# Performance work log

Measured on AMD Instinct MI355X. Metric: run time of the kernel, lower is better.

## Reference

```python
import jax, jax.numpy as jnp
import numpy as np

N = 262144      # total line-graph nodes (16 graphs x 16384)
E = 2097152     # total line-graph edges (avg degree 8)
F_IN = 8        # edge_attr feature dim
FEATURES_DIM = 64


def gcn_conv(x, src, dst, W, b, n):
    """PyG GCNConv: x' = D^{-1/2} (A+I) D^{-1/2} (x W) + b, deg from in-edges incl. self-loops."""
    x = x @ W
    loop = jnp.arange(n, dtype=src.dtype)
    si = jnp.concatenate([src, loop])
    di = jnp.concatenate([dst, loop])
    deg = jax.ops.segment_sum(jnp.ones(si.shape[0], dtype=x.dtype), di, num_segments=n)
    dinv = jnp.where(deg > 0, deg ** -0.5, 0.0)
    norm = dinv[si] * dinv[di]                      # [E+N]
    msg = x[si] * norm[:, None]                     # gather + scale
    return jax.ops.segment_sum(msg, di, num_segments=n) + b


def setup_inputs() -> dict:
    key = jax.random.key(0)
    ks = jax.random.split(key, 10)

    def lin(k, fan_in, fan_out):
        return jax.random.normal(k, (fan_in, fan_out), jnp.float32) * (1.0 / np.sqrt(fan_in))

    return {
        "x": jax.random.normal(ks[0], (N, F_IN), jnp.float32),
        "W1": lin(ks[1], F_IN, 16), "b1": jnp.zeros((16,), jnp.float32),
        "W2": lin(ks[2], 16, 32),   "b2": jnp.zeros((32,), jnp.float32),
        "W3": lin(ks[3], 32, 64),   "b3": jnp.zeros((64,), jnp.float32),
        "Wfc": lin(ks[4], 64, FEATURES_DIM), "bfc": jnp.zeros((FEATURES_DIM,), jnp.float32),
        "edge_index": jax.random.randint(ks[5], (2, E), 0, N, dtype=jnp.int32),
        "batch_size": 16,
    }


def reference(x, W1, b1, W2, b2, W3, b3, Wfc, bfc, edge_index, batch_size):
    src, dst = edge_index[0], edge_index[1]
    n = x.shape[0]
    h = jax.nn.relu(gcn_conv(x, src, dst, W1, b1, n))
    h = jax.nn.relu(gcn_conv(h, src, dst, W2, b2, n))
    h = jax.nn.relu(gcn_conv(h, src, dst, W3, b3, n))
    out = h @ Wfc + bfc
    return out.reshape(batch_size, -1, FEATURES_DIM)
```

## Files before the change

kernel.cpp:

```cpp
#include <hip/hip_runtime.h>
#include <hip/hip_bf16.h>


#define NB   256
#define NPB  1024
#define TILE 4096
#define SRCMASK 0x3FFFFu

typedef _Float16 half8 __attribute__((ext_vector_type(8)));
typedef float float4v __attribute__((ext_vector_type(4)));

__device__ __forceinline__ unsigned pkh(float a, float b) {
    unsigned short ua = __builtin_bit_cast(unsigned short, (_Float16)a);
    unsigned short ub = __builtin_bit_cast(unsigned short, (_Float16)b);
    return (unsigned)ua | ((unsigned)ub << 16);
}
__device__ __forceinline__ float h_lo(unsigned u) {
    return (float)__builtin_bit_cast(_Float16, (unsigned short)(u & 0xFFFFu));
}
__device__ __forceinline__ float h_hi(unsigned u) {
    return (float)__builtin_bit_cast(_Float16, (unsigned short)(u >> 16));
}

#define UNPK8_ADD(A, u) \
    A##0 += h_lo(u.x); A##1 += h_hi(u.x); A##2 += h_lo(u.y); A##3 += h_hi(u.y); \
    A##4 += h_lo(u.z); A##5 += h_hi(u.z); A##6 += h_lo(u.w); A##7 += h_hi(u.w);

__global__ void hist_kernel(const int* __restrict__ dst, int* __restrict__ ghist,
                            int E, int shift) {
    __shared__ int h[NB];
    int tid = threadIdx.x;
    h[tid] = 0;
    __syncthreads();
    int base = blockIdx.x * TILE;
    int cnt = min(TILE, E - base);
    for (int i = tid; i < cnt; i += 256)
        atomicAdd(&h[dst[base + i] >> shift], 1);
    __syncthreads();
    int v = h[tid];
    if (v) atomicAdd(&ghist[tid], v);
}

__global__ void bscan_kernel(const int* __restrict__ ghist, int* __restrict__ bbase,
                             int* __restrict__ gcursor,
                             const float* __restrict__ W3, const float* __restrict__ Wf,
                             _Float16* __restrict__ w3f, _Float16* __restrict__ wff) {
    __shared__ int sh[NB];
    int tid = threadIdx.x;
    int v = ghist[tid];
    sh[tid] = v;
    __syncthreads();
    for (int o = 1; o < NB; o <<= 1) {
        int t = (tid >= o) ? sh[tid - o] : 0;
        __syncthreads();
        sh[tid] += t;
        __syncthreads();
    }
    int incl = sh[tid];
    bbase[tid] = incl - v;
    gcursor[tid] = incl - v;
    if (tid == NB - 1) bbase[NB] = incl;
    for (int i = tid; i < 32 * 64; i += NB) {
        int k = i >> 6, j = i & 63;
        w3f[(j >> 4) * 512 + (j & 15) * 32 + (k >> 3) * 8 + (k & 7)] = (_Float16)W3[i];
    }
    for (int i = tid; i < 64 * 64; i += NB) {
        int k = i >> 6, j = i & 63;
        wff[((k >> 5) * 4 + (j >> 4)) * 512 + (j & 15) * 32 + ((k >> 3) & 3) * 8 + (k & 7)]
            = (_Float16)Wf[i];
    }
}

__global__ void __launch_bounds__(256)
partition_kernel(const int* __restrict__ src, const int* __restrict__ dst,
                 int* __restrict__ gcursor, unsigned int* __restrict__ bedge,
                 int E, int shift, int mask) {
    __shared__ int h[NB], st[NB], gp[NB];
    __shared__ unsigned short rk[TILE];
    __shared__ int sd[TILE];
    __shared__ int ss[TILE];
    int tid = threadIdx.x;
    h[tid] = 0;
    __syncthreads();
    int base = blockIdx.x * TILE;
    int cnt = min(TILE, E - base);
    for (int i = tid; i < cnt; i += 256)
        rk[i] = (unsigned short)atomicAdd(&h[dst[base + i] >> shift], 1);
    __syncthreads();
    int hv = h[tid];
    st[tid] = hv;
    __syncthreads();
    for (int o = 1; o < NB; o <<= 1) {
        int t = (tid >= o) ? st[tid - o] : 0;
        __syncthreads();
        st[tid] += t;
        __syncthreads();
    }
    st[tid] -= hv;
    gp[tid] = hv ? atomicAdd(&gcursor[tid], hv) : 0;
    __syncthreads();
    for (int i = tid; i < cnt; i += 256) {
        int d = dst[base + i];
        int b = d >> shift;
        int pos = st[b] + rk[i];
        sd[pos] = d;
        ss[pos] = src[base + i];
    }
    __syncthreads();
    for (int i = tid; i < cnt; i += 256) {
        int d = sd[i];
        int b = d >> shift;
        int g = gp[b] + (i - st[b]);
        bedge[g] = (unsigned int)ss[i] | ((unsigned int)(d & mask) << 18);
    }
}

__global__ void __launch_bounds__(256)
build_kernel(const int* __restrict__ bbase, const unsigned int* __restrict__ bedge,
             const float* __restrict__ x,
             int* __restrict__ off, float* __restrict__ dinv, int* __restrict__ adj,
             _Float16* __restrict__ y0h) {
    __shared__ int deg1[NPB];
    __shared__ int cur[NPB];
    __shared__ int bs[256];
    int tid = threadIdx.x;
    int b = blockIdx.x;
    int s = bbase[b], e = bbase[b + 1];
    int base = tid * 4;
#pragma unroll
    for (int i = 0; i < 4; i++) deg1[base + i] = 0;
    __syncthreads();
    for (int i = s + tid; i < e; i += 256)
        atomicAdd(&deg1[bedge[i] >> 18], 1);
    __syncthreads();
    int d0 = deg1[base], d1 = deg1[base + 1], d2 = deg1[base + 2], d3 = deg1[base + 3];
    int th = d0 + d1 + d2 + d3;
    bs[tid] = th;
    __syncthreads();
    for (int o = 1; o < 256; o <<= 1) {
        int t = (tid >= o) ? bs[tid - o] : 0;
        __syncthreads();
        bs[tid] += t;
        __syncthreads();
    }
    int run = s + bs[tid] - th;
    int vb = b * NPB + base;
    off[vb]     = run; cur[base]     = run; dinv[vb]     = rsqrtf((float)(d0 + 1)); run += d0;
    off[vb + 1] = run; cur[base + 1] = run; dinv[vb + 1] = rsqrtf((float)(d1 + 1)); run += d1;
    off[vb + 2] = run; cur[base + 2] = run; dinv[vb + 2] = rsqrtf((float)(d2 + 1)); run += d2;
    off[vb + 3] = run; cur[base + 3] = run; dinv[vb + 3] = rsqrtf((float)(d3 + 1)); run += d3;
    if (b == NB - 1 && tid == 255) off[NB * NPB] = e;
    __syncthreads();
    for (int i = s + tid; i < e; i += 256) {
        unsigned int pk = bedge[i];
        int p = atomicAdd(&cur[pk >> 18], 1);
        adj[p] = (int)(pk & SRCMASK);
    }
    for (int i = tid; i < NPB; i += 256) {
        float dv = rsqrtf((float)(deg1[i] + 1));
        const float4* xr = (const float4*)x + (size_t)(b * NPB + i) * 2;
        float4 t0 = xr[0], t1 = xr[1];
        uint4 pk;
        pk.x = pkh(t0.x * dv, t0.y * dv); pk.y = pkh(t0.z * dv, t0.w * dv);
        pk.z = pkh(t1.x * dv, t1.y * dv); pk.w = pkh(t1.z * dv, t1.w * dv);
        ((uint4*)y0h)[(size_t)b * NPB + i] = pk;
    }
}

__global__ void __launch_bounds__(256)
aggt1_kernel(const _Float16* __restrict__ y0h, const int* __restrict__ off,
             const int* __restrict__ adj, const float* __restrict__ dinv,
             const float* __restrict__ W1, const float* __restrict__ b1,
             _Float16* __restrict__ y1h) {
    __shared__ float Ws[8 * 16];
    __shared__ float bsh[16];
    const int tid = threadIdx.x;
    if (tid < 128) Ws[tid] = W1[tid];
    if (tid < 16) bsh[tid] = b1[tid];
    const int vg = blockIdx.x * 256 + tid;
    const uint4* y4 = (const uint4*)y0h;
    int beg = off[vg], end = off[vg + 1];
    uint4 us = y4[vg];
    float a0 = h_lo(us.x), a1 = h_hi(us.x), a2 = h_lo(us.y), a3 = h_hi(us.y),
          a4 = h_lo(us.z), a5 = h_hi(us.z), a6 = h_lo(us.w), a7 = h_hi(us.w);
    float c0 = 0, c1 = 0, c2 = 0, c3 = 0, c4 = 0, c5 = 0, c6 = 0, c7 = 0;
    int e = beg;
    for (; e + 8 <= end; e += 8) {
        int s0 = adj[e], s1 = adj[e + 1], s2 = adj[e + 2], s3 = adj[e + 3];
        int s4 = adj[e + 4], s5 = adj[e + 5], s6 = adj[e + 6], s7 = adj[e + 7];
        uint4 u0 = y4[s0], u1 = y4[s1], u2 = y4[s2], u3 = y4[s3];
        uint4 u4 = y4[s4], u5 = y4[s5], u6 = y4[s6], u7 = y4[s7];
        UNPK8_ADD(a, u0) UNPK8_ADD(c, u1) UNPK8_ADD(a, u2) UNPK8_ADD(c, u3)
        UNPK8_ADD(a, u4) UNPK8_ADD(c, u5) UNPK8_ADD(a, u6) UNPK8_ADD(c, u7)
    }
    for (; e + 2 <= end; e += 2) {
        int s0 = adj[e], s1 = adj[e + 1];
        uint4 u0 = y4[s0], u1 = y4[s1];
        UNPK8_ADD(a, u0) UNPK8_ADD(c, u1)
    }
    if (e < end) {
        uint4 u0 = y4[adj[e]];
        UNPK8_ADD(a, u0)
    }
    float dv = dinv[vg];
    float in[8];
    in[0] = (a0 + c0) * dv; in[1] = (a1 + c1) * dv;
    in[2] = (a2 + c2) * dv; in[3] = (a3 + c3) * dv;
    in[4] = (a4 + c4) * dv; in[5] = (a5 + c5) * dv;
    in[6] = (a6 + c6) * dv; in[7] = (a7 + c7) * dv;
    __syncthreads();
    const float4* W4 = (const float4*)Ws;
    float o[16];
    {
        float4 b0 = ((const float4*)bsh)[0], b1v = ((const float4*)bsh)[1];
        float4 b2v = ((const float4*)bsh)[2], b3v = ((const float4*)bsh)[3];
        o[0] = b0.x; o[1] = b0.y; o[2] = b0.z; o[3] = b0.w;
        o[4] = b1v.x; o[5] = b1v.y; o[6] = b1v.z; o[7] = b1v.w;
        o[8] = b2v.x; o[9] = b2v.y; o[10] = b2v.z; o[11] = b2v.w;
        o[12] = b3v.x; o[13] = b3v.y; o[14] = b3v.z; o[15] = b3v.w;
    }
#pragma unroll
    for (int k = 0; k < 8; k++) {
        float xk = in[k];
        float4 w0 = W4[k * 4 + 0], w1 = W4[k * 4 + 1];
        float4 w2 = W4[k * 4 + 2], w3 = W4[k * 4 + 3];
        o[0] = fmaf(xk, w0.x, o[0]);  o[1] = fmaf(xk, w0.y, o[1]);
        o[2] = fmaf(xk, w0.z, o[2]);  o[3] = fmaf(xk, w0.w, o[3]);
        o[4] = fmaf(xk, w1.x, o[4]);  o[5] = fmaf(xk, w1.y, o[5]);
        o[6] = fmaf(xk, w1.z, o[6]);  o[7] = fmaf(xk, w1.w, o[7]);
        o[8] = fmaf(xk, w2.x, o[8]);  o[9] = fmaf(xk, w2.y, o[9]);
        o[10] = fmaf(xk, w2.z, o[10]); o[11] = fmaf(xk, w2.w, o[11]);
        o[12] = fmaf(xk, w3.x, o[12]); o[13] = fmaf(xk, w3.y, o[13]);
        o[14] = fmaf(xk, w3.z, o[14]); o[15] = fmaf(xk, w3.w, o[15]);
    }
    uint4 p0, p1;
    p0.x = pkh(dv * fmaxf(o[0], 0.f),  dv * fmaxf(o[1], 0.f));
    p0.y = pkh(dv * fmaxf(o[2], 0.f),  dv * fmaxf(o[3], 0.f));
    p0.z = pkh(dv * fmaxf(o[4], 0.f),  dv * fmaxf(o[5], 0.f));
    p0.w = pkh(dv * fmaxf(o[6], 0.f),  dv * fmaxf(o[7], 0.f));
    p1.x = pkh(dv * fmaxf(o[8], 0.f),  dv * fmaxf(o[9], 0.f));
    p1.y = pkh(dv * fmaxf(o[10], 0.f), dv * fmaxf(o[11], 0.f));
    p1.z = pkh(dv * fmaxf(o[12], 0.f), dv * fmaxf(o[13], 0.f));
    p1.w = pkh(dv * fmaxf(o[14], 0.f), dv * fmaxf(o[15], 0.f));
    uint4* out4 = (uint4*)y1h;
    out4[(size_t)vg * 2]     = p0;
    out4[(size_t)vg * 2 + 1] = p1;
}

__global__ void __launch_bounds__(256)
aggt2_kernel(const _Float16* __restrict__ y1h, const int* __restrict__ off,
             const int* __restrict__ adj, const float* __restrict__ dinv,
             const float* __restrict__ W2, const float* __restrict__ b2,
             unsigned int* __restrict__ y2b) {
    __shared__ float Ws[16 * 32];
    __shared__ float bsh[32];
    const int tid = threadIdx.x;
    for (int i = tid; i < 16 * 32; i += 256) Ws[i] = W2[i];
    if (tid < 32) bsh[tid] = b2[tid];
    const int vbase = blockIdx.x * 128;
    const int vl = tid >> 1, c = tid & 1;
    const int vg = vbase + vl;
    const uint4* y4 = (const uint4*)y1h;
    int beg = off[vg], end = off[vg + 1];
    uint4 us = y4[(size_t)vg * 2 + c];
    float a0 = h_lo(us.x), a1 = h_hi(us.x), a2 = h_lo(us.y), a3 = h_hi(us.y),
          a4 = h_lo(us.z), a5 = h_hi(us.z), a6 = h_lo(us.w), a7 = h_hi(us.w);
    float c0 = 0, c1 = 0, c2 = 0, c3 = 0, c4 = 0, c5 = 0, c6 = 0, c7 = 0;
    int e = beg;
    for (; e + 8 <= end; e += 8) {
        int s0 = adj[e], s1 = adj[e + 1], s2 = adj[e + 2], s3 = adj[e + 3];
        int s4 = adj[e + 4], s5 = adj[e + 5], s6 = adj[e + 6], s7 = adj[e + 7];
        uint4 u0 = y4[(size_t)s0 * 2 + c], u1 = y4[(size_t)s1 * 2 + c];
        uint4 u2 = y4[(size_t)s2 * 2 + c], u3 = y4[(size_t)s3 * 2 + c];
        uint4 u4 = y4[(size_t)s4 * 2 + c], u5 = y4[(size_t)s5 * 2 + c];
        uint4 u6 = y4[(size_t)s6 * 2 + c], u7 = y4[(size_t)s7 * 2 + c];
        UNPK8_ADD(a, u0) UNPK8_ADD(c, u1) UNPK8_ADD(a, u2) UNPK8_ADD(c, u3)
        UNPK8_ADD(a, u4) UNPK8_ADD(c, u5) UNPK8_ADD(a, u6) UNPK8_ADD(c, u7)
    }
    for (; e + 2 <= end; e += 2) {
        int s0 = adj[e], s1 = adj[e + 1];
        uint4 u0 = y4[(size_t)s0 * 2 + c], u1 = y4[(size_t)s1 * 2 + c];
        UNPK8_ADD(a, u0) UNPK8_ADD(c, u1)
    }
    if (e < end) {
        uint4 u0 = y4[(size_t)adj[e] * 2 + c];
        UNPK8_ADD(a, u0)
    }
    float dv = dinv[vg];
    float own[8];
    own[0] = (a0 + c0) * dv; own[1] = (a1 + c1) * dv;
    own[2] = (a2 + c2) * dv; own[3] = (a3 + c3) * dv;
    own[4] = (a4 + c4) * dv; own[5] = (a5 + c5) * dv;
    own[6] = (a6 + c6) * dv; own[7] = (a7 + c7) * dv;
    float oth[8];
#pragma unroll
    for (int k = 0; k < 8; k++) oth[k] = __shfl_xor(own[k], 1);
    float in[16];
#pragma unroll
    for (int k = 0; k < 8; k++) {
        in[c * 8 + k] = own[k];
        in[(1 - c) * 8 + k] = oth[k];
    }
    __syncthreads();
    const int j0 = c * 16;
    const float4* W4 = (const float4*)Ws;
    float o[16];
#pragma unroll
    for (int jj = 0; jj < 16; jj += 4) {
        float4 bv = *(const float4*)&bsh[j0 + jj];
        o[jj] = bv.x; o[jj + 1] = bv.y; o[jj + 2] = bv.z; o[jj + 3] = bv.w;
    }
#pragma unroll
    for (int k = 0; k < 16; k++) {
        float xk = in[k];
        float4 w0 = W4[k * 8 + c * 4 + 0], w1 = W4[k * 8 + c * 4 + 1];
        float4 w2 = W4[k * 8 + c * 4 + 2], w3 = W4[k * 8 + c * 4 + 3];
        o[0] = fmaf(xk, w0.x, o[0]);  o[1] = fmaf(xk, w0.y, o[1]);
        o[2] = fmaf(xk, w0.z, o[2]);  o[3] = fmaf(xk, w0.w, o[3]);
        o[4] = fmaf(xk, w1.x, o[4]);  o[5] = fmaf(xk, w1.y, o[5]);
        o[6] = fmaf(xk, w1.z, o[6]);  o[7] = fmaf(xk, w1.w, o[7]);
        o[8] = fmaf(xk, w2.x, o[8]);  o[9] = fmaf(xk, w2.y, o[9]);
        o[10] = fmaf(xk, w2.z, o[10]); o[11] = fmaf(xk, w2.w, o[11]);
        o[12] = fmaf(xk, w3.x, o[12]); o[13] = fmaf(xk, w3.y, o[13]);
        o[14] = fmaf(xk, w3.z, o[14]); o[15] = fmaf(xk, w3.w, o[15]);
    }
    uint4 p0, p1;
    p0.x = pkh(dv * fmaxf(o[0], 0.f),  dv * fmaxf(o[1], 0.f));
    p0.y = pkh(dv * fmaxf(o[2], 0.f),  dv * fmaxf(o[3], 0.f));
    p0.z = pkh(dv * fmaxf(o[4], 0.f),  dv * fmaxf(o[5], 0.f));
    p0.w = pkh(dv * fmaxf(o[6], 0.f),  dv * fmaxf(o[7], 0.f));
    p1.x = pkh(dv * fmaxf(o[8], 0.f),  dv * fmaxf(o[9], 0.f));
    p1.y = pkh(dv * fmaxf(o[10], 0.f), dv * fmaxf(o[11], 0.f));
    p1.z = pkh(dv * fmaxf(o[12], 0.f), dv * fmaxf(o[13], 0.f));
    p1.w = pkh(dv * fmaxf(o[14], 0.f), dv * fmaxf(o[15], 0.f));
    uint4* out4 = (uint4*)y2b;
    out4[(size_t)vg * 4 + c * 2]     = p0;
    out4[(size_t)vg * 4 + c * 2 + 1] = p1;
}

__global__ void __launch_bounds__(256)
agg3_kernel(const unsigned int* __restrict__ y2b, const int* __restrict__ off,
            const int* __restrict__ adj, const float* __restrict__ dinv,
            _Float16* __restrict__ a3out, int n) {
    int t = blockIdx.x * 256 + threadIdx.x;
    int v = t >> 2, c = t & 3;
    if (v >= n) return;
    const uint4* yb = (const uint4*)y2b;
    uint4 us = yb[(size_t)v * 4 + c];
    float a0 = h_lo(us.x), a1 = h_hi(us.x), a2 = h_lo(us.y), a3 = h_hi(us.y),
          a4 = h_lo(us.z), a5 = h_hi(us.z), a6 = h_lo(us.w), a7 = h_hi(us.w);
    float c0 = 0, c1 = 0, c2 = 0, c3 = 0, c4 = 0, c5 = 0, c6 = 0, c7 = 0;
    int beg = off[v], end = off[v + 1];
    int e = beg;
    for (; e + 4 <= end; e += 4) {
        int s0 = adj[e], s1 = adj[e + 1], s2 = adj[e + 2], s3 = adj[e + 3];
        uint4 u0 = yb[(size_t)s0 * 4 + c];
        uint4 u1 = yb[(size_t)s1 * 4 + c];
        uint4 u2 = yb[(size_t)s2 * 4 + c];
        uint4 u3 = yb[(size_t)s3 * 4 + c];
        UNPK8_ADD(a, u0) UNPK8_ADD(c, u1) UNPK8_ADD(a, u2) UNPK8_ADD(c, u3)
    }
    for (; e + 2 <= end; e += 2) {
        int s0 = adj[e], s1 = adj[e + 1];
        uint4 u0 = yb[(size_t)s0 * 4 + c];
        uint4 u1 = yb[(size_t)s1 * 4 + c];
        UNPK8_ADD(a, u0) UNPK8_ADD(c, u1)
    }
    if (e < end) {
        uint4 u0 = yb[(size_t)adj[e] * 4 + c];
        UNPK8_ADD(a, u0)
    }
    float dv = dinv[v];
    uint4 st;
    st.x = pkh((a0 + c0) * dv, (a1 + c1) * dv);
    st.y = pkh((a2 + c2) * dv, (a3 + c3) * dv);
    st.z = pkh((a4 + c4) * dv, (a5 + c5) * dv);
    st.w = pkh((a6 + c6) * dv, (a7 + c7) * dv);
    ((uint4*)a3out)[(size_t)v * 4 + c] = st;
}

__global__ void __launch_bounds__(256)
t3fc_kernel(const _Float16* __restrict__ a3h,
            const _Float16* __restrict__ w3f, const float* __restrict__ b3,
            const _Float16* __restrict__ wff, const float* __restrict__ bf,
            float* __restrict__ out) {
    __shared__ __align__(16) _Float16 tA[4][1024];
    const int tid = threadIdx.x;
    const int w = tid >> 6, l = tid & 63;
    const int lr = l & 15, lh = l >> 4;
    const int vbase = blockIdx.x * 64 + w * 16;
    const int fragoff = lr * 32 + lh * 8;

    half8 A1 = *(const half8*)(a3h + (size_t)(vbase + lr) * 32 + lh * 8);

    float4v c1[4];
#pragma unroll
    for (int nt = 0; nt < 4; nt++) {
        float bv = b3[nt * 16 + lr];
        float4v ci = {bv, bv, bv, bv};
        half8 B = *(const half8*)(w3f + nt * 512 + fragoff);
        c1[nt] = __builtin_amdgcn_mfma_f32_16x16x32_f16(A1, B, ci, 0, 0, 0);
    }

    _Float16* tw = tA[w];
#pragma unroll
    for (int nt = 0; nt < 4; nt++) {
        int k2 = nt * 16 + lr;
        int base = (k2 >> 5) * 512 + ((k2 >> 3) & 3) * 8 + (k2 & 7);
#pragma unroll
        for (int r = 0; r < 4; r++)
            tw[base + (lh * 4 + r) * 32] = (_Float16)fmaxf(c1[nt][r], 0.f);
    }

    float4v c2[4];
#pragma unroll
    for (int nt = 0; nt < 4; nt++) {
        float bv = bf[nt * 16 + lr];
        c2[nt] = (float4v){bv, bv, bv, bv};
    }
#pragma unroll
    for (int ks = 0; ks < 2; ks++) {
        half8 A2 = *(const half8*)(tw + ks * 512 + fragoff);
#pragma unroll
        for (int nt = 0; nt < 4; nt++) {
            half8 B = *(const half8*)(wff + (ks * 4 + nt) * 512 + fragoff);
            c2[nt] = __builtin_amdgcn_mfma_f32_16x16x32_f16(A2, B, c2[nt], 0, 0, 0);
        }
    }

#pragma unroll
    for (int nt = 0; nt < 4; nt++) {
#pragma unroll
        for (int r = 0; r < 4; r++)
            out[(size_t)(vbase + lh * 4 + r) * 64 + nt * 16 + lr] = c2[nt][r];
    }
}

extern "C" void kernel_launch(void* const* d_in, const int* in_sizes, int n_in,
                              void* d_out, int out_size, void* d_ws, size_t ws_size,
                              hipStream_t stream) {
    const float* x  = (const float*)d_in[0];
    const float* W1 = (const float*)d_in[1];
    const float* b1 = (const float*)d_in[2];
    const float* W2 = (const float*)d_in[3];
    const float* b2 = (const float*)d_in[4];
    const float* W3 = (const float*)d_in[5];
    const float* b3 = (const float*)d_in[6];
    const float* Wf = (const float*)d_in[7];
    const float* bf = (const float*)d_in[8];
    const int*   ei = (const int*)d_in[9];

    const int N = in_sizes[0] / 8;
    const int E = in_sizes[9] / 2;
    const int* srcv = ei;
    const int* dstv = ei + E;
    const int shift = 10;

    char* p = (char*)d_ws;
    auto take = [&p](size_t bytes) { char* q = p; p += (bytes + 63) & ~size_t(63); return q; };
    int*   off   = (int*)take((size_t)(N + 16) * 4);
    float* dinv  = (float*)take((size_t)N * 4);
    int*   adj   = (int*)take((size_t)E * 4);
    int*   ghist = (int*)take(NB * 4);
    int*   bbase = (int*)take((NB + 1) * 4);
    int*   gcur  = (int*)take(NB * 4);
    _Float16* w3f = (_Float16*)take(32 * 64 * 2);
    _Float16* wff = (_Float16*)take(64 * 64 * 2);
    char*  bufA  = take((size_t)N * 32 * 4);
    char*  bufB  = take((size_t)N * 16 * 4);
    char*  regX  = take((size_t)N * 32 * 2);
    unsigned int* bedge = (unsigned int*)regX;
    unsigned int* y2b   = (unsigned int*)regX;
    _Float16* y0h = (_Float16*)bufA;
    _Float16* a3h = (_Float16*)bufA;
    _Float16* y1h = (_Float16*)bufB;

    hipMemsetAsync(ghist, 0, NB * 4, stream);

    int nt = (E + TILE - 1) / TILE;
    hist_kernel<<<nt, 256, 0, stream>>>(dstv, ghist, E, shift);
    bscan_kernel<<<1, NB, 0, stream>>>(ghist, bbase, gcur, W3, Wf, w3f, wff);
    partition_kernel<<<nt, 256, 0, stream>>>(srcv, dstv, gcur, bedge, E, shift, NPB - 1);
    build_kernel<<<NB, 256, 0, stream>>>(bbase, bedge, x, off, dinv, adj, y0h);

    aggt1_kernel<<<N / 256, 256, 0, stream>>>(y0h, off, adj, dinv, W1, b1, y1h);
    aggt2_kernel<<<N / 128, 256, 0, stream>>>(y1h, off, adj, dinv, W2, b2, y2b);
    agg3_kernel<<<(N * 4) / 256, 256, 0, stream>>>(y2b, off, adj, dinv, a3h, N);
    t3fc_kernel<<<N / 64, 256, 0, stream>>>(a3h, w3f, b3, wff, bf, (float*)d_out);
}
```

Before: 283.0 us.

## Sort nodes by in-degree to balance aggregation work across wavefront lanes

Builds a degree histogram during CSR construction, scans it, and scatters a degree-sorted permutation of nodes along with permuted offsets and dinv. The three aggregation kernels and the final MLP kernel then process nodes in degree order, so lanes in a wavefront run loops of similar length and diverge less. In exchange it adds two small kernels, extra indirection through perm, and scattered output writes. Reads of each node's own features also become non-contiguous.

```diff
diff --git a/kernel.cpp b/kernel.cpp
--- a/kernel.cpp
+++ b/kernel.cpp
@@ -6,6 +6,7 @@
 #define NPB  1024
 #define TILE 4096
 #define SRCMASK 0x3FFFFu
+#define DB   64
 
 typedef _Float16 half8 __attribute__((ext_vector_type(8)));
 typedef float float4v __attribute__((ext_vector_type(4)));
@@ -42,11 +43,12 @@
 }
 
 __global__ void bscan_kernel(const int* __restrict__ ghist, int* __restrict__ bbase,
-                             int* __restrict__ gcursor,
+                             int* __restrict__ gcursor, int* __restrict__ dhist,
                              const float* __restrict__ W3, const float* __restrict__ Wf,
                              _Float16* __restrict__ w3f, _Float16* __restrict__ wff) {
     __shared__ int sh[NB];
     int tid = threadIdx.x;
+    if (tid < DB) dhist[tid] = 0;
     int v = ghist[tid];
     sh[tid] = v;
     __syncthreads();
@@ -119,21 +121,25 @@
 build_kernel(const int* __restrict__ bbase, const unsigned int* __restrict__ bedge,
              const float* __restrict__ x,
              int* __restrict__ off, float* __restrict__ dinv, int* __restrict__ adj,
-             _Float16* __restrict__ y0h) {
+             _Float16* __restrict__ y0h, int* __restrict__ dhist) {
     __shared__ int deg1[NPB];
     __shared__ int cur[NPB];
     __shared__ int bs[256];
+    __shared__ int dh[DB];
     int tid = threadIdx.x;
     int b = blockIdx.x;
     int s = bbase[b], e = bbase[b + 1];
     int base = tid * 4;
 #pragma unroll
     for (int i = 0; i < 4; i++) deg1[base + i] = 0;
+    if (tid < DB) dh[tid] = 0;
     __syncthreads();
     for (int i = s + tid; i < e; i += 256)
         atomicAdd(&deg1[bedge[i] >> 18], 1);
     __syncthreads();
     int d0 = deg1[base], d1 = deg1[base + 1], d2 = deg1[base + 2], d3 = deg1[base + 3];
+    atomicAdd(&dh[min(d0, DB - 1)], 1); atomicAdd(&dh[min(d1, DB - 1)], 1);
+    atomicAdd(&dh[min(d2, DB - 1)], 1); atomicAdd(&dh[min(d3, DB - 1)], 1);
     int th = d0 + d1 + d2 + d3;
     bs[tid] = th;
     __syncthreads();
@@ -150,6 +156,7 @@
     off[vb + 2] = run; cur[base + 2] = run; dinv[vb + 2] = rsqrtf((float)(d2 + 1)); run += d2;
     off[vb + 3] = run; cur[base + 3] = run; dinv[vb + 3] = rsqrtf((float)(d3 + 1)); run += d3;
     if (b == NB - 1 && tid == 255) off[NB * NPB] = e;
+    if (tid < DB && dh[tid]) atomicAdd(&dhist[tid], dh[tid]);
     __syncthreads();
     for (int i = s + tid; i < e; i += 256) {
         unsigned int pk = bedge[i];
@@ -167,9 +174,55 @@
     }
 }
 
-__global__ void __launch_bounds__(256)
-aggt1_kernel(const _Float16* __restrict__ y0h, const int* __restrict__ off,
-             const int* __restrict__ adj, const float* __restrict__ dinv,
+__global__ void dscan_kernel(const int* __restrict__ dhist, int* __restrict__ dcur) {
+    __shared__ int sh[DB];
+    int tid = threadIdx.x;
+    int v = dhist[tid];
+    sh[tid] = v;
+    __syncthreads();
+    for (int o = 1; o < DB; o <<= 1) {
+        int t = (tid >= o) ? sh[tid - o] : 0;
+        __syncthreads();
+        sh[tid] += t;
+        __syncthreads();
+    }
+    dcur[tid] = sh[tid] - v;
+}
+
+__global__ void __launch_bounds__(256)
+dscatter_kernel(const int* __restrict__ off, const float* __restrict__ dinv,
+                int* __restrict__ dcur, int* __restrict__ perm,
+                uint2* __restrict__ offp, float* __restrict__ dinvp) {
+    __shared__ unsigned short rk[1024];
+    __shared__ unsigned char dgs[1024];
+    __shared__ int lh[DB], gb[DB];
+    const int tid = threadIdx.x;
+    const int vb = blockIdx.x * 1024;
+    if (tid < DB) lh[tid] = 0;
+    __syncthreads();
+    for (int ln = tid; ln < 1024; ln += 256) {
+        int v = vb + ln;
+        int d = min(off[v + 1] - off[v], DB - 1);
+        dgs[ln] = (unsigned char)d;
+        rk[ln] = (unsigned short)atomicAdd(&lh[d], 1);
+    }
+    __syncthreads();
+    if (tid < DB) gb[tid] = lh[tid] ? atomicAdd(&dcur[tid], lh[tid]) : 0;
+    __syncthreads();
+    for (int ln = tid; ln < 1024; ln += 256) {
+        int v = vb + ln;
+        int g = gb[dgs[ln]] + rk[ln];
+        perm[g] = v;
+        uint2 oo; oo.x = (unsigned)off[v]; oo.y = (unsigned)off[v + 1];
+        offp[g] = oo;
+        dinvp[g] = dinv[v];
+    }
+}
+
+__global__ void __launch_bounds__(256)
+aggt1_kernel(const _Float16* __restrict__ y0h, const uint2* __restrict__ offp,
+             const int* __restrict__ adj, const float* __restrict__ dinvp,
+             const int* __restrict__ perm,
              const float* __restrict__ W1, const float* __restrict__ b1,
              _Float16* __restrict__ y1h) {
     __shared__ float Ws[8 * 16];
@@ -177,10 +230,12 @@
     const int tid = threadIdx.x;
     if (tid < 128) Ws[tid] = W1[tid];
     if (tid < 16) bsh[tid] = b1[tid];
-    const int vg = blockIdx.x * 256 + tid;
+    const int r = blockIdx.x * 256 + tid;
+    const int pv = perm[r];
+    const uint2 oo = offp[r];
     const uint4* y4 = (const uint4*)y0h;
-    int beg = off[vg], end = off[vg + 1];
-    uint4 us = y4[vg];
+    int beg = (int)oo.x, end = (int)oo.y;
+    uint4 us = y4[pv];
     float a0 = h_lo(us.x), a1 = h_hi(us.x), a2 = h_lo(us.y), a3 = h_hi(us.y),
           a4 = h_lo(us.z), a5 = h_hi(us.z), a6 = h_lo(us.w), a7 = h_hi(us.w);
     float c0 = 0, c1 = 0, c2 = 0, c3 = 0, c4 = 0, c5 = 0, c6 = 0, c7 = 0;
@@ -202,7 +257,7 @@
         uint4 u0 = y4[adj[e]];
         UNPK8_ADD(a, u0)
     }
-    float dv = dinv[vg];
+    float dv = dinvp[r];
     float in[8];
     in[0] = (a0 + c0) * dv; in[1] = (a1 + c1) * dv;
     in[2] = (a2 + c2) * dv; in[3] = (a3 + c3) * dv;
@@ -243,13 +298,14 @@
     p1.z = pkh(dv * fmaxf(o[12], 0.f), dv * fmaxf(o[13], 0.f));
     p1.w = pkh(dv * fmaxf(o[14], 0.f), dv * fmaxf(o[15], 0.f));
     uint4* out4 = (uint4*)y1h;
-    out4[(size_t)vg * 2]     = p0;
-    out4[(size_t)vg * 2 + 1] = p1;
-}
-
-__global__ void __launch_bounds__(256)
-aggt2_kernel(const _Float16* __restrict__ y1h, const int* __restrict__ off,
-             const int* __restrict__ adj, const float* __restrict__ dinv,
+    out4[(size_t)pv * 2]     = p0;
+    out4[(size_t)pv * 2 + 1] = p1;
+}
+
+__global__ void __launch_bounds__(256)
+aggt2_kernel(const _Float16* __restrict__ y1h, const uint2* __restrict__ offp,
+             const int* __restrict__ adj, const float* __restrict__ dinvp,
+             const int* __restrict__ perm,
              const float* __restrict__ W2, const float* __restrict__ b2,
              unsigned int* __restrict__ y2b) {
     __shared__ float Ws[16 * 32];
@@ -257,12 +313,13 @@
     const int tid = threadIdx.x;
     for (int i = tid; i < 16 * 32; i += 256) Ws[i] = W2[i];
     if (tid < 32) bsh[tid] = b2[tid];
-    const int vbase = blockIdx.x * 128;
     const int vl = tid >> 1, c = tid & 1;
-    const int vg = vbase + vl;
+    const int r = blockIdx.x * 128 + vl;
+    const int pv = perm[r];
+    const uint2 oo = offp[r];
     const uint4* y4 = (const uint4*)y1h;
-    int beg = off[vg], end = off[vg + 1];
-    uint4 us = y4[(size_t)vg * 2 + c];
+    int beg = (int)oo.x, end = (int)oo.y;
+    uint4 us = y4[(size_t)pv * 2 + c];
     float a0 = h_lo(us.x), a1 = h_hi(us.x), a2 = h_lo(us.y), a3 = h_hi(us.y),
           a4 = h_lo(us.z), a5 = h_hi(us.z), a6 = h_lo(us.w), a7 = h_hi(us.w);
     float c0 = 0, c1 = 0, c2 = 0, c3 = 0, c4 = 0, c5 = 0, c6 = 0, c7 = 0;
@@ -286,7 +343,7 @@
         uint4 u0 = y4[(size_t)adj[e] * 2 + c];
         UNPK8_ADD(a, u0)
     }
-    float dv = dinv[vg];
+    float dv = dinvp[r];
     float own[8];
     own[0] = (a0 + c0) * dv; own[1] = (a1 + c1) * dv;
     own[2] = (a2 + c2) * dv; own[3] = (a3 + c3) * dv;
@@ -334,23 +391,26 @@
     p1.z = pkh(dv * fmaxf(o[12], 0.f), dv * fmaxf(o[13], 0.f));
     p1.w = pkh(dv * fmaxf(o[14], 0.f), dv * fmaxf(o[15], 0.f));
     uint4* out4 = (uint4*)y2b;
-    out4[(size_t)vg * 4 + c * 2]     = p0;
-    out4[(size_t)vg * 4 + c * 2 + 1] = p1;
-}
-
-__global__ void __launch_bounds__(256)
-agg3_kernel(const unsigned int* __restrict__ y2b, const int* __restrict__ off,
-            const int* __restrict__ adj, const float* __restrict__ dinv,
+    out4[(size_t)pv * 4 + c * 2]     = p0;
+    out4[(size_t)pv * 4 + c * 2 + 1] = p1;
+}
+
+__global__ void __launch_bounds__(256)
+agg3_kernel(const unsigned int* __restrict__ y2b, const uint2* __restrict__ offp,
+            const int* __restrict__ adj, const float* __restrict__ dinvp,
+            const int* __restrict__ perm,
             _Float16* __restrict__ a3out, int n) {
     int t = blockIdx.x * 256 + threadIdx.x;
-    int v = t >> 2, c = t & 3;
-    if (v >= n) return;
+    int r = t >> 2, c = t & 3;
+    if (r >= n) return;
+    const int pv = perm[r];
+    const uint2 oo = offp[r];
     const uint4* yb = (const uint4*)y2b;
-    uint4 us = yb[(size_t)v * 4 + c];
+    uint4 us = yb[(size_t)pv * 4 + c];
     float a0 = h_lo(us.x), a1 = h_hi(us.x), a2 = h_lo(us.y), a3 = h_hi(us.y),
           a4 = h_lo(us.z), a5 = h_hi(us.z), a6 = h_lo(us.w), a7 = h_hi(us.w);
     float c0 = 0, c1 = 0, c2 = 0, c3 = 0, c4 = 0, c5 = 0, c6 = 0, c7 = 0;
-    int beg = off[v], end = off[v + 1];
+    int beg = (int)oo.x, end = (int)oo.y;
     int e = beg;
     for (; e + 4 <= end; e += 4) {
         int s0 = adj[e], s1 = adj[e + 1], s2 = adj[e + 2], s3 = adj[e + 3];
@@ -370,17 +430,17 @@
         uint4 u0 = yb[(size_t)adj[e] * 4 + c];
         UNPK8_ADD(a, u0)
     }
-    float dv = dinv[v];
+    float dv = dinvp[r];
     uint4 st;
     st.x = pkh((a0 + c0) * dv, (a1 + c1) * dv);
     st.y = pkh((a2 + c2) * dv, (a3 + c3) * dv);
     st.z = pkh((a4 + c4) * dv, (a5 + c5) * dv);
     st.w = pkh((a6 + c6) * dv, (a7 + c7) * dv);
-    ((uint4*)a3out)[(size_t)v * 4 + c] = st;
-}
-
-__global__ void __launch_bounds__(256)
-t3fc_kernel(const _Float16* __restrict__ a3h,
+    ((uint4*)a3out)[(size_t)r * 4 + c] = st;
+}
+
+__global__ void __launch_bounds__(256)
+t3fc_kernel(const _Float16* __restrict__ a3h, const int* __restrict__ perm,
             const _Float16* __restrict__ w3f, const float* __restrict__ b3,
             const _Float16* __restrict__ wff, const float* __restrict__ bf,
             float* __restrict__ out) {
@@ -408,8 +468,8 @@
         int k2 = nt * 16 + lr;
         int base = (k2 >> 5) * 512 + ((k2 >> 3) & 3) * 8 + (k2 & 7);
 #pragma unroll
-        for (int r = 0; r < 4; r++)
-            tw[base + (lh * 4 + r) * 32] = (_Float16)fmaxf(c1[nt][r], 0.f);
+        for (int rr = 0; rr < 4; rr++)
+            tw[base + (lh * 4 + rr) * 32] = (_Float16)fmaxf(c1[nt][rr], 0.f);
     }
 
     float4v c2[4];
@@ -428,11 +488,14 @@
         }
     }
 
+    int pr[4];
+#pragma unroll
+    for (int rr = 0; rr < 4; rr++) pr[rr] = perm[vbase + lh * 4 + rr];
 #pragma unroll
     for (int nt = 0; nt < 4; nt++) {
 #pragma unroll
-        for (int r = 0; r < 4; r++)
-            out[(size_t)(vbase + lh * 4 + r) * 64 + nt * 16 + lr] = c2[nt][r];
+        for (int rr = 0; rr < 4; rr++)
+            out[(size_t)pr[rr] * 64 + nt * 16 + lr] = c2[nt][rr];
     }
 }
 
@@ -464,6 +527,11 @@
     int*   ghist = (int*)take(NB * 4);
     int*   bbase = (int*)take((NB + 1) * 4);
     int*   gcur  = (int*)take(NB * 4);
+    int*   dhist = (int*)take(DB * 4);
+    int*   dcur  = (int*)take(DB * 4);
+    int*   perm  = (int*)take((size_t)N * 4);
+    uint2* offp  = (uint2*)take((size_t)N * 8);
+    float* dinvp = (float*)take((size_t)N * 4);
     _Float16* w3f = (_Float16*)take(32 * 64 * 2);
     _Float16* wff = (_Float16*)take(64 * 64 * 2);
     char*  bufA  = take((size_t)N * 32 * 4);
@@ -479,12 +547,14 @@
 
     int nt = (E + TILE - 1) / TILE;
     hist_kernel<<<nt, 256, 0, stream>>>(dstv, ghist, E, shift);
-    bscan_kernel<<<1, NB, 0, stream>>>(ghist, bbase, gcur, W3, Wf, w3f, wff);
+    bscan_kernel<<<1, NB, 0, stream>>>(ghist, bbase, gcur, dhist, W3, Wf, w3f, wff);
     partition_kernel<<<nt, 256, 0, stream>>>(srcv, dstv, gcur, bedge, E, shift, NPB - 1);
-    build_kernel<<<NB, 256, 0, stream>>>(bbase, bedge, x, off, dinv, adj, y0h);
-
-    aggt1_kernel<<<N / 256, 256, 0, stream>>>(y0h, off, adj, dinv, W1, b1, y1h);
-    aggt2_kernel<<<N / 128, 256, 0, stream>>>(y1h, off, adj, dinv, W2, b2, y2b);
-    agg3_kernel<<<(N * 4) / 256, 256, 0, stream>>>(y2b, off, adj, dinv, a3h, N);
-    t3fc_kernel<<<N / 64, 256, 0, stream>>>(a3h, w3f, b3, wff, bf, (float*)d_out);
-}
+    build_kernel<<<NB, 256, 0, stream>>>(bbase, bedge, x, off, dinv, adj, y0h, dhist);
+    dscan_kernel<<<1, DB, 0, stream>>>(dhist, dcur);
+    dscatter_kernel<<<N / 1024, 256, 0, stream>>>(off, dinv, dcur, perm, offp, dinvp);
+
+    aggt1_kernel<<<N / 256, 256, 0, stream>>>(y0h, offp, adj, dinvp, perm, W1, b1, y1h);
+    aggt2_kernel<<<N / 128, 256, 0, stream>>>(y1h, offp, adj, dinvp, perm, W2, b2, y2b);
+    agg3_kernel<<<(N * 4) / 256, 256, 0, stream>>>(y2b, offp, adj, dinvp, perm, a3h, N);
+    t3fc_kernel<<<N / 64, 256, 0, stream>>>(a3h, perm, w3f, b3, wff, bf, (float*)d_out);
+}
```

Measured after the change: 319.9 us. 13.0% more time.

## Split layer-2 aggregation into two half-feature passes with nontemporal index loads

Applied to the files above, without the earlier changes.

Layer-1 output is stored as two separate 8-half planes instead of one interleaved 16-half row. Layer-2 aggregation is split into two kernels, each gathering one plane with one thread per node. The first writes fp32 partial sums to a scratch buffer and the second combines them and applies W2. Each gather pass now touches a smaller working set that fits better in cache. The adjacency reads and several stores are made nontemporal to avoid polluting cache. The cost is a second pass over adj and an extra fp32 partial-sum round trip through memory.

```diff
diff --git a/kernel.cpp b/kernel.cpp
--- a/kernel.cpp
+++ b/kernel.cpp
@@ -9,6 +9,7 @@
 
 typedef _Float16 half8 __attribute__((ext_vector_type(8)));
 typedef float float4v __attribute__((ext_vector_type(4)));
+typedef unsigned int u32x4 __attribute__((ext_vector_type(4)));
 
 __device__ __forceinline__ unsigned pkh(float a, float b) {
     unsigned short ua = __builtin_bit_cast(unsigned short, (_Float16)a);
@@ -21,6 +22,7 @@
 __device__ __forceinline__ float h_hi(unsigned u) {
     return (float)__builtin_bit_cast(_Float16, (unsigned short)(u >> 16));
 }
+__device__ __forceinline__ int ld_nt(const int* p) { return __builtin_nontemporal_load(p); }
 
 #define UNPK8_ADD(A, u) \
     A##0 += h_lo(u.x); A##1 += h_hi(u.x); A##2 += h_lo(u.y); A##3 += h_hi(u.y); \
@@ -171,35 +173,37 @@
 aggt1_kernel(const _Float16* __restrict__ y0h, const int* __restrict__ off,
              const int* __restrict__ adj, const float* __restrict__ dinv,
              const float* __restrict__ W1, const float* __restrict__ b1,
-             _Float16* __restrict__ y1h) {
+             _Float16* __restrict__ y1a, _Float16* __restrict__ y1b) {
     __shared__ float Ws[8 * 16];
     __shared__ float bsh[16];
     const int tid = threadIdx.x;
     if (tid < 128) Ws[tid] = W1[tid];
     if (tid < 16) bsh[tid] = b1[tid];
     const int vg = blockIdx.x * 256 + tid;
-    const uint4* y4 = (const uint4*)y0h;
+    const u32x4* y4 = (const u32x4*)y0h;
     int beg = off[vg], end = off[vg + 1];
-    uint4 us = y4[vg];
+    u32x4 us = y4[vg];
     float a0 = h_lo(us.x), a1 = h_hi(us.x), a2 = h_lo(us.y), a3 = h_hi(us.y),
           a4 = h_lo(us.z), a5 = h_hi(us.z), a6 = h_lo(us.w), a7 = h_hi(us.w);
     float c0 = 0, c1 = 0, c2 = 0, c3 = 0, c4 = 0, c5 = 0, c6 = 0, c7 = 0;
     int e = beg;
     for (; e + 8 <= end; e += 8) {
-        int s0 = adj[e], s1 = adj[e + 1], s2 = adj[e + 2], s3 = adj[e + 3];
-        int s4 = adj[e + 4], s5 = adj[e + 5], s6 = adj[e + 6], s7 = adj[e + 7];
-        uint4 u0 = y4[s0], u1 = y4[s1], u2 = y4[s2], u3 = y4[s3];
-        uint4 u4 = y4[s4], u5 = y4[s5], u6 = y4[s6], u7 = y4[s7];
+        int s0 = ld_nt(adj + e),     s1 = ld_nt(adj + e + 1);
+        int s2 = ld_nt(adj + e + 2), s3 = ld_nt(adj + e + 3);
+        int s4 = ld_nt(adj + e + 4), s5 = ld_nt(adj + e + 5);
+        int s6 = ld_nt(adj + e + 6), s7 = ld_nt(adj + e + 7);
+        u32x4 u0 = y4[s0], u1 = y4[s1], u2 = y4[s2], u3 = y4[s3];
+        u32x4 u4 = y4[s4], u5 = y4[s5], u6 = y4[s6], u7 = y4[s7];
         UNPK8_ADD(a, u0) UNPK8_ADD(c, u1) UNPK8_ADD(a, u2) UNPK8_ADD(c, u3)
         UNPK8_ADD(a, u4) UNPK8_ADD(c, u5) UNPK8_ADD(a, u6) UNPK8_ADD(c, u7)
     }
     for (; e + 2 <= end; e += 2) {
-        int s0 = adj[e], s1 = adj[e + 1];
-        uint4 u0 = y4[s0], u1 = y4[s1];
+        int s0 = ld_nt(adj + e), s1 = ld_nt(adj + e + 1);
+        u32x4 u0 = y4[s0], u1 = y4[s1];
         UNPK8_ADD(a, u0) UNPK8_ADD(c, u1)
     }
     if (e < end) {
-        uint4 u0 = y4[adj[e]];
+        u32x4 u0 = y4[ld_nt(adj + e)];
         UNPK8_ADD(a, u0)
     }
     float dv = dinv[vg];
@@ -233,7 +237,7 @@
         o[12] = fmaf(xk, w3.x, o[12]); o[13] = fmaf(xk, w3.y, o[13]);
         o[14] = fmaf(xk, w3.z, o[14]); o[15] = fmaf(xk, w3.w, o[15]);
     }
-    uint4 p0, p1;
+    u32x4 p0, p1;
     p0.x = pkh(dv * fmaxf(o[0], 0.f),  dv * fmaxf(o[1], 0.f));
     p0.y = pkh(dv * fmaxf(o[2], 0.f),  dv * fmaxf(o[3], 0.f));
     p0.z = pkh(dv * fmaxf(o[4], 0.f),  dv * fmaxf(o[5], 0.f));
@@ -242,100 +246,124 @@
     p1.y = pkh(dv * fmaxf(o[10], 0.f), dv * fmaxf(o[11], 0.f));
     p1.z = pkh(dv * fmaxf(o[12], 0.f), dv * fmaxf(o[13], 0.f));
     p1.w = pkh(dv * fmaxf(o[14], 0.f), dv * fmaxf(o[15], 0.f));
-    uint4* out4 = (uint4*)y1h;
-    out4[(size_t)vg * 2]     = p0;
-    out4[(size_t)vg * 2 + 1] = p1;
-}
-
-__global__ void __launch_bounds__(256)
-aggt2_kernel(const _Float16* __restrict__ y1h, const int* __restrict__ off,
-             const int* __restrict__ adj, const float* __restrict__ dinv,
-             const float* __restrict__ W2, const float* __restrict__ b2,
-             unsigned int* __restrict__ y2b) {
+    __builtin_nontemporal_store(p0, (u32x4*)y1a + vg);
+    __builtin_nontemporal_store(p1, (u32x4*)y1b + vg);
+}
+
+__global__ void __launch_bounds__(256)
+aggt2a_kernel(const _Float16* __restrict__ y1a, const int* __restrict__ off,
+              const int* __restrict__ adj, float* __restrict__ P) {
+    const int vg = blockIdx.x * 256 + threadIdx.x;
+    const u32x4* y4 = (const u32x4*)y1a;
+    int beg = off[vg], end = off[vg + 1];
+    u32x4 us = y4[vg];
+    float a0 = h_lo(us.x), a1 = h_hi(us.x), a2 = h_lo(us.y), a3 = h_hi(us.y),
+          a4 = h_lo(us.z), a5 = h_hi(us.z), a6 = h_lo(us.w), a7 = h_hi(us.w);
+    float c0 = 0, c1 = 0, c2 = 0, c3 = 0, c4 = 0, c5 = 0, c6 = 0, c7 = 0;
+    int e = beg;
+    for (; e + 8 <= end; e += 8) {
+        int s0 = ld_nt(adj + e),     s1 = ld_nt(adj + e + 1);
+        int s2 = ld_nt(adj + e + 2), s3 = ld_nt(adj + e + 3);
+        int s4 = ld_nt(adj + e + 4), s5 = ld_nt(adj + e + 5);
+        int s6 = ld_nt(adj + e + 6), s7 = ld_nt(adj + e + 7);
+        u32x4 u0 = y4[s0], u1 = y4[s1], u2 = y4[s2], u3 = y4[s3];
+        u32x4 u4 = y4[s4], u5 = y4[s5], u6 = y4[s6], u7 = y4[s7];
+        UNPK8_ADD(a, u0) UNPK8_ADD(c, u1) UNPK8_ADD(a, u2) UNPK8_ADD(c, u3)
+        UNPK8_ADD(a, u4) UNPK8_ADD(c, u5) UNPK8_ADD(a, u6) UNPK8_ADD(c, u7)
+    }
+    for (; e + 2 <= end; e += 2) {
+        int s0 = ld_nt(adj + e), s1 = ld_nt(adj + e + 1);
+        u32x4 u0 = y4[s0], u1 = y4[s1];
+        UNPK8_ADD(a, u0) UNPK8_ADD(c, u1)
+    }
+    if (e < end) {
+        u32x4 u0 = y4[ld_nt(adj + e)];
+        UNPK8_ADD(a, u0)
+    }
+    float4v q0 = {a0 + c0, a1 + c1, a2 + c2, a3 + c3};
+    float4v q1 = {a4 + c4, a5 + c5, a6 + c6, a7 + c7};
+    __builtin_nontemporal_store(q0, (float4v*)(P + (size_t)vg * 8));
+    __builtin_nontemporal_store(q1, (float4v*)(P + (size_t)vg * 8) + 1);
+}
+
+__global__ void __launch_bounds__(256)
+aggt2b_kernel(const _Float16* __restrict__ y1b, const int* __restrict__ off,
+              const int* __restrict__ adj, const float* __restrict__ dinv,
+              const float* __restrict__ P,
+              const float* __restrict__ W2, const float* __restrict__ b2,
+              unsigned int* __restrict__ y2b) {
     __shared__ float Ws[16 * 32];
     __shared__ float bsh[32];
     const int tid = threadIdx.x;
     for (int i = tid; i < 16 * 32; i += 256) Ws[i] = W2[i];
     if (tid < 32) bsh[tid] = b2[tid];
-    const int vbase = blockIdx.x * 128;
-    const int vl = tid >> 1, c = tid & 1;
-    const int vg = vbase + vl;
-    const uint4* y4 = (const uint4*)y1h;
+    const int vg = blockIdx.x * 256 + tid;
+    const u32x4* y4 = (const u32x4*)y1b;
     int beg = off[vg], end = off[vg + 1];
-    uint4 us = y4[(size_t)vg * 2 + c];
+    u32x4 us = y4[vg];
     float a0 = h_lo(us.x), a1 = h_hi(us.x), a2 = h_lo(us.y), a3 = h_hi(us.y),
           a4 = h_lo(us.z), a5 = h_hi(us.z), a6 = h_lo(us.w), a7 = h_hi(us.w);
     float c0 = 0, c1 = 0, c2 = 0, c3 = 0, c4 = 0, c5 = 0, c6 = 0, c7 = 0;
     int e = beg;
     for (; e + 8 <= end; e += 8) {
-        int s0 = adj[e], s1 = adj[e + 1], s2 = adj[e + 2], s3 = adj[e + 3];
-        int s4 = adj[e + 4], s5 = adj[e + 5], s6 = adj[e + 6], s7 = adj[e + 7];
-        uint4 u0 = y4[(size_t)s0 * 2 + c], u1 = y4[(size_t)s1 * 2 + c];
-        uint4 u2 = y4[(size_t)s2 * 2 + c], u3 = y4[(size_t)s3 * 2 + c];
-        uint4 u4 = y4[(size_t)s4 * 2 + c], u5 = y4[(size_t)s5 * 2 + c];
-        uint4 u6 = y4[(size_t)s6 * 2 + c], u7 = y4[(size_t)s7 * 2 + c];
+        int s0 = ld_nt(adj + e),     s1 = ld_nt(adj + e + 1);
+        int s2 = ld_nt(adj + e + 2), s3 = ld_nt(adj + e + 3);
+        int s4 = ld_nt(adj + e + 4), s5 = ld_nt(adj + e + 5);
+        int s6 = ld_nt(adj + e + 6), s7 = ld_nt(adj + e + 7);
+        u32x4 u0 = y4[s0], u1 = y4[s1], u2 = y4[s2], u3 = y4[s3];
+        u32x4 u4 = y4[s4], u5 = y4[s5], u6 = y4[s6], u7 = y4[s7];
         UNPK8_ADD(a, u0) UNPK8_ADD(c, u1) UNPK8_ADD(a, u2) UNPK8_ADD(c, u3)
         UNPK8_ADD(a, u4) UNPK8_ADD(c, u5) UNPK8_ADD(a, u6) UNPK8_ADD(c, u7)
     }
     for (; e + 2 <= end; e += 2) {
-        int s0 = adj[e], s1 = adj[e + 1];
-        uint4 u0 = y4[(size_t)s0 * 2 + c], u1 = y4[(size_t)s1 * 2 + c];
+        int s0 = ld_nt(adj + e), s1 = ld_nt(adj + e + 1);
+        u32x4 u0 = y4[s0], u1 = y4[s1];
         UNPK8_ADD(a, u0) UNPK8_ADD(c, u1)
     }
     if (e < end) {
-        uint4 u0 = y4[(size_t)adj[e] * 2 + c];
+        u32x4 u0 = y4[ld_nt(adj + e)];
         UNPK8_ADD(a, u0)
     }
     float dv = dinv[vg];
-    float own[8];
-    own[0] = (a0 + c0) * dv; own[1] = (a1 + c1) * dv;
-    own[2] = (a2 + c2) * dv; own[3] = (a3 + c3) * dv;
-    own[4] = (a4 + c4) * dv; own[5] = (a5 + c5) * dv;
-    own[6] = (a6 + c6) * dv; own[7] = (a7 + c7) * dv;
-    float oth[8];
-#pragma unroll
-    for (int k = 0; k < 8; k++) oth[k] = __shfl_xor(own[k], 1);
+    float4v q0 = __builtin_nontemporal_load((const float4v*)(P + (size_t)vg * 8));
+    float4v q1 = __builtin_nontemporal_load((const float4v*)(P + (size_t)vg * 8) + 1);
     float in[16];
-#pragma unroll
-    for (int k = 0; k < 8; k++) {
-        in[c * 8 + k] = own[k];
-        in[(1 - c) * 8 + k] = oth[k];
-    }
-    __syncthreads();
-    const int j0 = c * 16;
+    in[0] = q0.x * dv; in[1] = q0.y * dv; in[2] = q0.z * dv; in[3] = q0.w * dv;
+    in[4] = q1.x * dv; in[5] = q1.y * dv; in[6] = q1.z * dv; in[7] = q1.w * dv;
+    in[8]  = (a0 + c0) * dv; in[9]  = (a1 + c1) * dv;
+    in[10] = (a2 + c2) * dv; in[11] = (a3 + c3) * dv;
+    in[12] = (a4 + c4) * dv; in[13] = (a5 + c5) * dv;
+    in[14] = (a6 + c6) * dv; in[15] = (a7 + c7) * dv;
+    __syncthreads();
     const float4* W4 = (const float4*)Ws;
-    float o[16];
-#pragma unroll
-    for (int jj = 0; jj < 16; jj += 4) {
-        float4 bv = *(const float4*)&bsh[j0 + jj];
+    float o[32];
+#pragma unroll
+    for (int jj = 0; jj < 32; jj += 4) {
+        float4 bv = *(const float4*)&bsh[jj];
         o[jj] = bv.x; o[jj + 1] = bv.y; o[jj + 2] = bv.z; o[jj + 3] = bv.w;
     }
 #pragma unroll
     for (int k = 0; k < 16; k++) {
         float xk = in[k];
-        float4 w0 = W4[k * 8 + c * 4 + 0], w1 = W4[k * 8 + c * 4 + 1];
-        float4 w2 = W4[k * 8 + c * 4 + 2], w3 = W4[k * 8 + c * 4 + 3];
-        o[0] = fmaf(xk, w0.x, o[0]);  o[1] = fmaf(xk, w0.y, o[1]);
-        o[2] = fmaf(xk, w0.z, o[2]);  o[3] = fmaf(xk, w0.w, o[3]);
-        o[4] = fmaf(xk, w1.x, o[4]);  o[5] = fmaf(xk, w1.y, o[5]);
-        o[6] = fmaf(xk, w1.z, o[6]);  o[7] = fmaf(xk, w1.w, o[7]);
-        o[8] = fmaf(xk, w2.x, o[8]);  o[9] = fmaf(xk, w2.y, o[9]);
-        o[10] = fmaf(xk, w2.z, o[10]); o[11] = fmaf(xk, w2.w, o[11]);
-        o[12] = fmaf(xk, w3.x, o[12]); o[13] = fmaf(xk, w3.y, o[13]);
-        o[14] = fmaf(xk, w3.z, o[14]); o[15] = fmaf(xk, w3.w, o[15]);
-    }
-    uint4 p0, p1;
-    p0.x = pkh(dv * fmaxf(o[0], 0.f),  dv * fmaxf(o[1], 0.f));
-    p0.y = pkh(dv * fmaxf(o[2], 0.f),  dv * fmaxf(o[3], 0.f));
-    p0.z = pkh(dv * fmaxf(o[4], 0.f),  dv * fmaxf(o[5], 0.f));
-    p0.w = pkh(dv * fmaxf(o[6], 0.f),  dv * fmaxf(o[7], 0.f));
-    p1.x = pkh(dv * fmaxf(o[8], 0.f),  dv * fmaxf(o[9], 0.f));
-    p1.y = pkh(dv * fmaxf(o[10], 0.f), dv * fmaxf(o[11], 0.f));
-    p1.z = pkh(dv * fmaxf(o[12], 0.f), dv * fmaxf(o[13], 0.f));
-    p1.w = pkh(dv * fmaxf(o[14], 0.f), dv * fmaxf(o[15], 0.f));
-    uint4* out4 = (uint4*)y2b;
-    out4[(size_t)vg * 4 + c * 2]     = p0;
-    out4[(size_t)vg * 4 + c * 2 + 1] = p1;
+#pragma unroll
+        for (int q = 0; q < 8; q++) {
+            float4 w = W4[k * 8 + q];
+            o[q * 4 + 0] = fmaf(xk, w.x, o[q * 4 + 0]);
+            o[q * 4 + 1] = fmaf(xk, w.y, o[q * 4 + 1]);
+            o[q * 4 + 2] = fmaf(xk, w.z, o[q * 4 + 2]);
+            o[q * 4 + 3] = fmaf(xk, w.w, o[q * 4 + 3]);
+        }
+    }
+    u32x4* out4 = (u32x4*)y2b + (size_t)vg * 4;
+#pragma unroll
+    for (int q = 0; q < 4; q++) {
+        u32x4 pk;
+        pk.x = pkh(dv * fmaxf(o[q * 8 + 0], 0.f), dv * fmaxf(o[q * 8 + 1], 0.f));
+        pk.y = pkh(dv * fmaxf(o[q * 8 + 2], 0.f), dv * fmaxf(o[q * 8 + 3], 0.f));
+        pk.z = pkh(dv * fmaxf(o[q * 8 + 4], 0.f), dv * fmaxf(o[q * 8 + 5], 0.f));
+        pk.w = pkh(dv * fmaxf(o[q * 8 + 6], 0.f), dv * fmaxf(o[q * 8 + 7], 0.f));
+        __builtin_nontemporal_store(pk, out4 + q);
+    }
 }
 
 __global__ void __launch_bounds__(256)
@@ -345,38 +373,39 @@
     int t = blockIdx.x * 256 + threadIdx.x;
     int v = t >> 2, c = t & 3;
     if (v >= n) return;
-    const uint4* yb = (const uint4*)y2b;
-    uint4 us = yb[(size_t)v * 4 + c];
+    const u32x4* yb = (const u32x4*)y2b;
+    u32x4 us = yb[(size_t)v * 4 + c];
     float a0 = h_lo(us.x), a1 = h_hi(us.x), a2 = h_lo(us.y), a3 = h_hi(us.y),
           a4 = h_lo(us.z), a5 = h_hi(us.z), a6 = h_lo(us.w), a7 = h_hi(us.w);
     float c0 = 0, c1 = 0, c2 = 0, c3 = 0, c4 = 0, c5 = 0, c6 = 0, c7 = 0;
     int beg = off[v], end = off[v + 1];
     int e = beg;
     for (; e + 4 <= end; e += 4) {
-        int s0 = adj[e], s1 = adj[e + 1], s2 = adj[e + 2], s3 = adj[e + 3];
-        uint4 u0 = yb[(size_t)s0 * 4 + c];
-        uint4 u1 = yb[(size_t)s1 * 4 + c];
-        uint4 u2 = yb[(size_t)s2 * 4 + c];
-        uint4 u3 = yb[(size_t)s3 * 4 + c];
+        int s0 = ld_nt(adj + e),     s1 = ld_nt(adj + e + 1);
+        int s2 = ld_nt(adj + e + 2), s3 = ld_nt(adj + e + 3);
+        u32x4 u0 = yb[(size_t)s0 * 4 + c];
+        u32x4 u1 = yb[(size_t)s1 * 4 + c];
+        u32x4 u2 = yb[(size_t)s2 * 4 + c];
+        u32x4 u3 = yb[(size_t)s3 * 4 + c];
         UNPK8_ADD(a, u0) UNPK8_ADD(c, u1) UNPK8_ADD(a, u2) UNPK8_ADD(c, u3)
     }
     for (; e + 2 <= end; e += 2) {
-        int s0 = adj[e], s1 = adj[e + 1];
-        uint4 u0 = yb[(size_t)s0 * 4 + c];
-        uint4 u1 = yb[(size_t)s1 * 4 + c];
+        int s0 = ld_nt(adj + e), s1 = ld_nt(adj + e + 1);
+        u32x4 u0 = yb[(size_t)s0 * 4 + c];
+        u32x4 u1 = yb[(size_t)s1 * 4 + c];
         UNPK8_ADD(a, u0) UNPK8_ADD(c, u1)
     }
     if (e < end) {
-        uint4 u0 = yb[(size_t)adj[e] * 4 + c];
+        u32x4 u0 = yb[(size_t)ld_nt(adj + e) * 4 + c];
         UNPK8_ADD(a, u0)
     }
     float dv = dinv[v];
-    uint4 st;
+    u32x4 st;
     st.x = pkh((a0 + c0) * dv, (a1 + c1) * dv);
     st.y = pkh((a2 + c2) * dv, (a3 + c3) * dv);
     st.z = pkh((a4 + c4) * dv, (a5 + c5) * dv);
     st.w = pkh((a6 + c6) * dv, (a7 + c7) * dv);
-    ((uint4*)a3out)[(size_t)v * 4 + c] = st;
+    ((u32x4*)a3out)[(size_t)v * 4 + c] = st;
 }
 
 __global__ void __launch_bounds__(256)
@@ -473,7 +502,9 @@
     unsigned int* y2b   = (unsigned int*)regX;
     _Float16* y0h = (_Float16*)bufA;
     _Float16* a3h = (_Float16*)bufA;
-    _Float16* y1h = (_Float16*)bufB;
+    _Float16* y1a = (_Float16*)bufB;
+    _Float16* y1b = (_Float16*)(bufB + (size_t)N * 16);
+    float*    Ppart = (float*)(bufB + (size_t)N * 32);
 
     hipMemsetAsync(ghist, 0, NB * 4, stream);
 
@@ -483,8 +514,9 @@
     partition_kernel<<<nt, 256, 0, stream>>>(srcv, dstv, gcur, bedge, E, shift, NPB - 1);
     build_kernel<<<NB, 256, 0, stream>>>(bbase, bedge, x, off, dinv, adj, y0h);
 
-    aggt1_kernel<<<N / 256, 256, 0, stream>>>(y0h, off, adj, dinv, W1, b1, y1h);
-    aggt2_kernel<<<N / 128, 256, 0, stream>>>(y1h, off, adj, dinv, W2, b2, y2b);
+    aggt1_kernel<<<N / 256, 256, 0, stream>>>(y0h, off, adj, dinv, W1, b1, y1a, y1b);
+    aggt2a_kernel<<<N / 256, 256, 0, stream>>>(y1a, off, adj, Ppart);
+    aggt2b_kernel<<<N / 256, 256, 0, stream>>>(y1b, off, adj, dinv, Ppart, W2, b2, y2b);
     agg3_kernel<<<(N * 4) / 256, 256, 0, stream>>>(y2b, off, adj, dinv, a3h, N);
     t3fc_kernel<<<N / 64, 256, 0, stream>>>(a3h, w3f, b3, wff, bf, (float*)d_out);
 }
```

After: 300.4 us. 1.06x slower.
